# Kernel optimization log

Hardware: AMD Instinct MI355X
Metric: run time of the kernel (lower is better)

The kernel has to match this reference:

```python
import jax, jax.numpy as jnp
import numpy as np
import math

NUM_CLASSES = 80
ANCHORS = [(12.0, 16.0), (19.0, 36.0), (40.0, 28.0)]
ANGLES = [-np.pi/3, -np.pi/6, 0.0, np.pi/6, np.pi/3, np.pi/2]
STRIDE = 8.0
SCALE_XY = 1.05
IGNORE_THRESH = 0.5
MASKED_ANCHORS = np.array([[w/STRIDE, h/STRIDE, a] for (w, h) in ANCHORS for a in ANGLES], dtype=np.float32)  # [18,3]
NA = MASKED_ANCHORS.shape[0]
LAMBDA_COORD, LAMBDA_CONF, LAMBDA_CLS = 1.0, 10.0, 1.0
FOCAL_ALPHA, FOCAL_GAMMA = 0.25, 2.0


def setup_inputs() -> dict:
    key = jax.random.key(0)
    B, G, nT = 8, 76, 240
    k1, k2, k3, k4, k5, k6 = jax.random.split(key, 6)
    output = jax.random.normal(k1, (B, NA * (NUM_CLASSES + 6), G, G), jnp.float32) * 0.1
    tb = jax.random.randint(k2, (nT,), 0, B).astype(jnp.float32)
    tl = jax.random.randint(k3, (nT,), 0, NUM_CLASSES).astype(jnp.float32)
    txy = jax.random.uniform(k4, (nT, 2), minval=0.02, maxval=0.98)
    twh = jax.random.uniform(k5, (nT, 2), minval=0.05, maxval=0.4)
    tang = jax.random.uniform(k6, (nT, 1), minval=-np.pi/2, maxval=np.pi/2)
    target = jnp.concatenate([tb[:, None], tl[:, None], txy, twh, tang], axis=-1)  # [nT,7]
    return {"output": output, "target": target}


def _smooth_l1(x, y):
    d = jnp.abs(x - y)
    return jnp.where(d < 1.0, 0.5 * d * d, d - 0.5)


def _bce(p, t):
    eps = 1e-7
    p = jnp.clip(p, eps, 1.0 - eps)
    return -(t * jnp.log(p) + (1.0 - t) * jnp.log(1.0 - p))


def _focal(p, t):
    loss = _bce(p, t)
    p_t = t * p + (1.0 - t) * (1.0 - p)
    alpha_f = t * FOCAL_ALPHA + (1.0 - t) * (1.0 - FOCAL_ALPHA)
    return loss * alpha_f * (1.0 - p_t) ** FOCAL_GAMMA


def _ciou(pb, tb):
    # pb, tb: [N,5] (cx, cy, w, h, angle) in grid units
    p1, p2 = pb[:, :2] - pb[:, 2:4] / 2, pb[:, :2] + pb[:, 2:4] / 2
    t1, t2 = tb[:, :2] - tb[:, 2:4] / 2, tb[:, :2] + tb[:, 2:4] / 2
    w1, h1 = p2[:, 0] - p1[:, 0], p2[:, 1] - p1[:, 1]
    w2, h2 = t2[:, 0] - t1[:, 0], t2[:, 1] - t1[:, 1]
    area1, area2 = w1 * h1, w2 * h2
    c1, c2 = (p1 + p2) / 2, (t1 + t2) / 2
    inter = jnp.clip(jnp.minimum(p2, t2) - jnp.maximum(p1, t1), 0.0)
    inter_area = inter[:, 0] * inter[:, 1]
    inter_diag = jnp.sum((c2 - c1) ** 2, axis=-1)
    outer = jnp.clip(jnp.maximum(p2, t2) - jnp.minimum(p1, t1), 0.0)
    outer_diag = outer[:, 0] ** 2 + outer[:, 1] ** 2
    union = area1 + area2 - inter_area
    u = inter_diag / outer_diag
    iou = inter_area / union
    v = (4.0 / math.pi ** 2) * (jnp.arctan(w2 / h2) - jnp.arctan(w1 / h1)) ** 2
    alpha = jax.lax.stop_gradient(v / ((1.0 - iou) + v))
    ciou = jnp.clip(iou - (u + alpha * v), -1.0, 1.0)
    skew_iou = iou * jnp.abs(jnp.cos(pb[:, 4] - tb[:, 4]))
    return skew_iou, ciou


def _forward(output, target):
    B, G = output.shape[0], output.shape[2]
    nC = NUM_CLASSES
    ma = jnp.asarray(MASKED_ANCHORS)
    pred = output.reshape(B, NA, nC + 6, G, G).transpose(0, 1, 3, 4, 2)  # [B,A,G,G,C+6]
    px = jax.nn.sigmoid(pred[..., 0]) * SCALE_XY - (SCALE_XY - 1) / 2
    py = jax.nn.sigmoid(pred[..., 1]) * SCALE_XY - (SCALE_XY - 1) / 2
    pw, ph, pa = pred[..., 2], pred[..., 3], pred[..., 4]
    pconf = jax.nn.sigmoid(pred[..., 5])
    pcls = jax.nn.sigmoid(pred[..., 6:])
    gx = jnp.arange(G, dtype=output.dtype)[None, None, None, :]
    gy = jnp.arange(G, dtype=output.dtype)[None, None, :, None]
    aw = ma[:, 0].reshape(1, NA, 1, 1)
    ah = ma[:, 1].reshape(1, NA, 1, 1)
    aa = ma[:, 2].reshape(1, NA, 1, 1)
    pred_boxes = jnp.stack([px + gx, py + gy, jnp.exp(pw) * aw, jnp.exp(ph) * ah, pa + aa], axis=-1)  # [B,A,G,G,5]
    out_dec = jnp.concatenate([
        jnp.concatenate([pred_boxes[..., :4] * STRIDE, pred_boxes[..., 4:]], axis=-1).reshape(B, -1, 5),
        pconf.reshape(B, -1, 1),
        pcls.reshape(B, -1, nC)], axis=-1)

    # ---- build_targets ----
    tgt_boxes = jnp.concatenate([target[:, 2:6] * G, target[:, 6:]], axis=-1)  # [nT,5]
    gxy, gwh, ga = tgt_boxes[:, :2], tgt_boxes[:, 2:4], tgt_boxes[:, 4]
    aw_, ah_, aa_ = ma[:, 0][:, None], ma[:, 1][:, None], ma[:, 2][:, None]  # [A,1]
    w2, h2 = gwh[:, 0][None, :], gwh[:, 1][None, :]                          # [1,nT]
    inter = jnp.minimum(aw_, w2) * jnp.minimum(ah_, h2)
    union = aw_ * ah_ + 1e-16 + w2 * h2 - inter
    offset = jnp.abs(aa_ - ga[None, :])                                       # [A,nT]
    arious = (inter / union) * jnp.abs(jnp.cos(aa_ - ga[None, :]))            # [A,nT]
    best_n = jnp.argmax(arious, axis=0)                                       # [nT]
    b = target[:, 0].astype(jnp.int32)
    labels = target[:, 1].astype(jnp.int32)
    gi = gxy[:, 0].astype(jnp.int32)
    gj = gxy[:, 1].astype(jnp.int32)

    zeros = jnp.zeros((B, NA, G, G), output.dtype)
    obj = zeros.at[b, best_n, gj, gi].set(1.0)
    noobj = jnp.ones((B, NA, G, G), output.dtype)
    cond = (arious > IGNORE_THRESH) | ((arious > 0.4) & (offset < np.pi / 12))  # [A,nT]
    a_idx = jnp.broadcast_to(jnp.arange(NA)[:, None], arious.shape)
    bb = jnp.broadcast_to(b[None, :], arious.shape)
    gjb = jnp.broadcast_to(gj[None, :], arious.shape)
    gib = jnp.broadcast_to(gi[None, :], arious.shape)
    noobj = noobj.at[bb, a_idx, gjb, gib].min(jnp.where(cond, 0.0, 1.0))
    noobj = noobj.at[b, best_n, gj, gi].set(0.0)

    ta_grid = zeros.at[b, best_n, gj, gi].set(ga - ma[best_n, 2])
    tcls = jnp.zeros((B, NA, G, G, nC), output.dtype).at[b, best_n, gj, gi, labels].set(1.0)
    tconf = obj

    pb = pred_boxes[b, best_n, gj, gi]  # [nT,5]
    iou, ciou = _ciou(pb, tgt_boxes)
    img_size = STRIDE * G
    bbox_scale = jax.lax.stop_gradient(2.0 - gwh[:, 0] * gwh[:, 1] / img_size ** 2)
    ciou_t = bbox_scale * (1.0 - ciou)

    class_ok = (jnp.argmax(pcls[b, best_n, gj, gi], axis=-1) == labels).astype(output.dtype)
    class_mask = zeros.at[b, best_n, gj, gi].set(class_ok)
    iou_scores = zeros.at[b, best_n, gj, gi].set(iou)
    skew = zeros.at[b, best_n, gj, gi].set(jnp.exp(1.0 - iou) - 1.0)
    ciou_grid = zeros.at[b, best_n, gj, gi].set(ciou_t)

    # ---- losses (masked means replace boolean indexing) ----
    n_obj = jnp.maximum(jnp.sum(obj), 1.0)
    n_noobj = jnp.maximum(jnp.sum(noobj), 1.0)
    reg = _smooth_l1(pa, ta_grid) + ciou_grid
    reg_const = jax.lax.stop_gradient(skew / jnp.where(obj > 0, reg, 1.0))
    reg_loss = jnp.sum(reg * reg_const * obj) / n_obj
    fl = _focal(pconf, tconf)
    conf_loss = jnp.sum(fl * obj) / n_obj + jnp.sum(fl * noobj) / n_noobj
    cls_loss = jnp.sum(_bce(pcls, tcls) * obj[..., None]) / (n_obj * nC)
    total_loss = LAMBDA_COORD * reg_loss + LAMBDA_CONF * conf_loss + LAMBDA_CLS * cls_loss
    return out_dec, total_loss


def reference(output, target):
    return _forward(output, target)
```

## Files before the change

### kernel.cpp

```cpp
#include <hip/hip_runtime.h>
#include <math.h>

#define NCLS 80
#define NANC 18
#define NB 8
#define GG 76
#define SS (GG*GG)
#define CHN (NCLS+6)
#define NCELL (NB*NANC*SS)
#define FLAG_WORDS ((NCELL+31)/32)
#define NT_MAX 240
#define TILE 76
#define LSTR 77
#define TPB 4
#define TGRP (GG/TPB)
#define THR 512
#define NLOAD 4
#define TOT4 (CHN*(TILE/4))
#define NCONF4 (NCELL/4)
#define NCONFBLK ((NCONF4+255)/256)
#define PI_ 3.14159265358979323846

#define WS_WIN   64
#define WS_META  1024
#define WS_LM    4864
#define WS_FLAGS 6784

__device__ __constant__ float d_ma[NANC][3] = {
  {1.5f, 2.0f, (float)(-PI_/3)}, {1.5f, 2.0f, (float)(-PI_/6)}, {1.5f, 2.0f, 0.0f},
  {1.5f, 2.0f, (float)(PI_/6)},  {1.5f, 2.0f, (float)(PI_/3)},  {1.5f, 2.0f, (float)(PI_/2)},
  {2.375f, 4.5f, (float)(-PI_/3)}, {2.375f, 4.5f, (float)(-PI_/6)}, {2.375f, 4.5f, 0.0f},
  {2.375f, 4.5f, (float)(PI_/6)},  {2.375f, 4.5f, (float)(PI_/3)},  {2.375f, 4.5f, (float)(PI_/2)},
  {5.0f, 3.5f, (float)(-PI_/3)}, {5.0f, 3.5f, (float)(-PI_/6)}, {5.0f, 3.5f, 0.0f},
  {5.0f, 3.5f, (float)(PI_/6)},  {5.0f, 3.5f, (float)(PI_/3)},  {5.0f, 3.5f, (float)(PI_/2)},
};

__device__ __forceinline__ float sigm(float x) { return 1.0f / (1.0f + expf(-x)); }
__device__ __forceinline__ float fsig(float x) {
  return __builtin_amdgcn_rcpf(1.0f + __expf(-x));
}

__global__ __launch_bounds__(256) void k_prep(const float* __restrict__ tgt,
                                              unsigned* __restrict__ flags,
                                              int* __restrict__ win,
                                              int4* __restrict__ meta,
                                              uint2* __restrict__ lmout,
                                              int* __restrict__ cnt,
                                              double* __restrict__ acc, int nT) {
  __shared__ int s_key[NT_MAX], s_lab[NT_MAX];
  __shared__ int s_win[NT_MAX];
  __shared__ int s_zero;

  int t = threadIdx.x;
  uint4* f4 = (uint4*)flags;
  for (int i = t; i < FLAG_WORDS/4; i += 256) f4[i] = make_uint4(0,0,0,0);
  if (t < 4) { acc[t] = 0.0; cnt[t] = 0; }
  if (t == 0) s_zero = 0;
  __syncthreads();

  int bi = 0, gi = 0, gj = 0, bn = 0;
  unsigned cm = 0;
  if (t < nT) {
    float bf = tgt[t*7+0], lf = tgt[t*7+1];
    float gx = tgt[t*7+2] * (float)GG, gy = tgt[t*7+3] * (float)GG;
    float gw = tgt[t*7+4] * (float)GG, gh = tgt[t*7+5] * (float)GG;
    float ga = tgt[t*7+6];
    bi = (int)bf; gi = (int)gx; gj = (int)gy;
    int lab = (int)lf;
    float best = -1e30f;
    for (int a = 0; a < NANC; ++a) {
      float aw = d_ma[a][0], ah = d_ma[a][1], aa = d_ma[a][2];
      float inter = fminf(aw, gw) * fminf(ah, gh);
      float uni = aw*ah + 1e-16f + gw*gh - inter;
      float off = fabsf(aa - ga);
      float ar = inter / uni * fabsf(cosf(aa - ga));
      if (ar > best) { best = ar; bn = a; }
      if (ar > 0.5f || (ar > 0.4f && off < (float)(PI_/12))) cm |= (1u << a);
    }
    s_key[t] = ((bi*NANC + bn)*GG + gj)*GG + gi;
    s_lab[t] = lab;
    s_win[t] = 0;
  }
  __syncthreads();

  if (t < nT) {
    for (int a = 0; a < NANC; ++a) {
      if (((cm >> a) & 1u) || a == bn) {
        int cell = ((bi*NANC + a)*GG + gj)*GG + gi;
        unsigned bit = 1u << (cell & 31);
        unsigned old = atomicOr(&flags[cell >> 5], bit);
        if (!(old & bit)) atomicAdd(&s_zero, 1);
      }
    }
    int key = s_key[t];
    bool winner = true;
    for (int t2 = t + 1; t2 < nT; ++t2) if (s_key[t2] == key) { winner = false; break; }
    if (winner) {
      s_win[t] = 1;
      unsigned long long lm0 = 0, lm1 = 0;
      for (int t2 = 0; t2 < nT; ++t2) if (s_key[t2] == key) {
        int L = s_lab[t2];
        if (L < 64) lm0 |= 1ull << L; else lm1 |= 1ull << (L - 64);
      }
      lmout[t] = make_uint2((unsigned)(lm0 & 0xffffffffull), (unsigned)(lm0 >> 32));
      meta[t] = make_int4(bi, bn, gi, gj | ((int)(lm1 & 0xffffu) << 16));
      win[t] = 1;
    } else {
      win[t] = 0;
    }
  }
  __syncthreads();
  if (t == 0) {
    int nw = 0;
    for (int i = 0; i < nT; ++i) nw += s_win[i];
    cnt[0] = s_zero; cnt[1] = nw;
  }
}

__global__ __launch_bounds__(256) void k_loss(const float* __restrict__ tgt,
                                              const float* __restrict__ in,
                                              const int* __restrict__ win,
                                              const int4* __restrict__ meta,
                                              const uint2* __restrict__ lm,
                                              const unsigned* __restrict__ flags,
                                              double* __restrict__ acc,
                                              int* __restrict__ cnt,
                                              float* __restrict__ out, int nT) {
  int blk = blockIdx.x;
  int tid = threadIdx.x;
  int nblk = nT + NCONFBLK;

  if (blk < nT) {
    if (win[blk]) {
      int t = blk;
      int4 m = meta[t];
      int bi = m.x, bn = m.y, gi = m.z, gj = m.w & 0xffff;
      unsigned lmhi = ((unsigned)m.w) >> 16;
      uint2 l0 = lm[t];
      const float* base = in + ((size_t)(bi*NANC + bn)*CHN)*SS + (size_t)gj*GG + gi;

      float csum = 0.0f;
      if (tid < NCLS) {
        float p = fsig(base[(size_t)(6 + tid)*SS]);
        float pl = fminf(fmaxf(p, 1e-7f), 1.0f - 1e-7f);
        bool tc;
        if (tid < 32)      tc = (l0.x >> tid) & 1u;
        else if (tid < 64) tc = (l0.y >> (tid - 32)) & 1u;
        else               tc = (lmhi >> (tid - 64)) & 1u;
        csum = tc ? -__logf(pl) : -__logf(1.0f - pl);
      }
      for (int off = 32; off; off >>= 1) csum += __shfl_down(csum, off);
      if ((tid & 63) == 0 && tid < 128) atomicAdd(&acc[3], (double)csum);

      if (tid == 128) {
        float gx = tgt[t*7+2] * (float)GG, gyv = tgt[t*7+3] * (float)GG;
        float gw = tgt[t*7+4] * (float)GG, gh = tgt[t*7+5] * (float)GG;
        float ga = tgt[t*7+6];
        float rx = base[0], ry = base[(size_t)SS], rw = base[2*(size_t)SS],
              rh = base[3*(size_t)SS], ra = base[4*(size_t)SS], rcf = base[5*(size_t)SS];
        float aw = d_ma[bn][0], ah = d_ma[bn][1], aa = d_ma[bn][2];
        float px = sigm(rx)*1.05f - 0.025f + (float)gi;
        float py = sigm(ry)*1.05f - 0.025f + (float)gj;
        float pw = expf(rw)*aw, ph = expf(rh)*ah;
        float pang = ra + aa;
        float p1x = px - pw*0.5f, p1y = py - ph*0.5f, p2x = px + pw*0.5f, p2y = py + ph*0.5f;
        float t1x = gx - gw*0.5f, t1y = gyv - gh*0.5f, t2x = gx + gw*0.5f, t2y = gyv + gh*0.5f;
        float w1 = p2x - p1x, h1 = p2y - p1y, w2 = t2x - t1x, h2 = t2y - t1y;
        float area1 = w1*h1, area2 = w2*h2;
        float c1x = (p1x+p2x)*0.5f, c1y = (p1y+p2y)*0.5f, c2x = (t1x+t2x)*0.5f, c2y = (t1y+t2y)*0.5f;
        float ix = fmaxf(fminf(p2x,t2x) - fmaxf(p1x,t1x), 0.0f);
        float iy = fmaxf(fminf(p2y,t2y) - fmaxf(p1y,t1y), 0.0f);
        float inter_area = ix*iy;
        float dcx = c2x - c1x, dcy = c2y - c1y;
        float inter_diag = dcx*dcx + dcy*dcy;
        float ox = fmaxf(fmaxf(p2x,t2x) - fminf(p1x,t1x), 0.0f);
        float oy = fmaxf(fmaxf(p2y,t2y) - fminf(p1y,t1y), 0.0f);
        float outer_diag = ox*ox + oy*oy;
        float uni = area1 + area2 - inter_area;
        float u = inter_diag / outer_diag;
        float iou = inter_area / uni;
        float da = atanf(w2/h2) - atanf(w1/h1);
        float v = (float)(4.0/(PI_*PI_)) * da * da;
        float alpha = v / (1.0f - iou + v);
        float ciou = fminf(fmaxf(iou - (u + alpha*v), -1.0f), 1.0f);
        float skew_iou = iou * fabsf(cosf(pang - ga));
        float skew = expf(1.0f - skew_iou) - 1.0f;
        float bscale = 2.0f - gw*gh/369664.0f;
        float ciou_t = bscale * (1.0f - ciou);
        float ta = ga - aa;
        float d = fabsf(ra - ta);
        float sl1 = (d < 1.0f) ? 0.5f*d*d : d - 0.5f;
        float reg = sl1 + ciou_t;
        atomicAdd(&acc[2], (double)(reg * (skew / reg)));
        float pc = sigm(rcf);
        float pcl = fminf(fmaxf(pc, 1e-7f), 1.0f - 1e-7f);
        float om = 1.0f - pc;
        atomicAdd(&acc[1], (double)(-logf(pcl) * 0.25f * om * om));
      }
    }
  } else {
    __shared__ double wsum[4];
    int j = (blk - nT)*256 + tid;
    double fl = 0.0;
    if (j < NCONF4) {
      int ba = j / (SS/4);
      int q  = j - ba*(SS/4);
      int spos = 4*q;
      const float4 v4 = *(const float4*)(in + (size_t)ba*CHN*SS + 5*(size_t)SS + spos);
      int cell0 = ba*SS + spos;
      unsigned word = flags[cell0 >> 5];
      int bbit = cell0 & 31;
      float pv[4] = {v4.x, v4.y, v4.z, v4.w};
      #pragma unroll
      for (int e = 0; e < 4; ++e) {
        if (!((word >> (bbit + e)) & 1u)) {
          float p = fsig(pv[e]);
          float pcl = fminf(fmaxf(p, 1e-7f), 1.0f - 1e-7f);
          fl += (double)(-__logf(1.0f - pcl) * 0.75f * p * p);
        }
      }
    }
    int lane = tid & 63, wid = tid >> 6;
    for (int off = 32; off; off >>= 1) fl += __shfl_down(fl, off);
    if (lane == 0) wsum[wid] = fl;
    __syncthreads();
    if (tid == 0) {
      double s = wsum[0] + wsum[1] + wsum[2] + wsum[3];
      if (s != 0.0) atomicAdd(&acc[0], s);
    }
  }

  __syncthreads();
  if (tid == 0) {
    __threadfence();
    unsigned tk = atomicAdd((unsigned*)&cnt[2], 1u);
    if (tk == (unsigned)(nblk - 1)) {
      double a0 = atomicAdd(&acc[0], 0.0);
      double a1 = atomicAdd(&acc[1], 0.0);
      double a2 = atomicAdd(&acc[2], 0.0);
      double a3 = atomicAdd(&acc[3], 0.0);
      int c0 = atomicAdd(&cnt[0], 0);
      int c1 = atomicAdd(&cnt[1], 0);
      double n_obj = fmax((double)c1, 1.0);
      double n_noobj = fmax((double)(NCELL - c0), 1.0);
      double loss = a2/n_obj + 10.0*(a1/n_obj + a0/n_noobj) + a3/(n_obj*(double)NCLS);
      out[(size_t)NCELL*CHN] = (float)loss;
    }
  }
}

__global__ __launch_bounds__(THR) void k_main(const float* __restrict__ in,
                                              float* __restrict__ out) {
  __shared__ float lds[CHN * LSTR];
  int blk = blockIdx.x;
  int tgrp = blk % TGRP;
  int ba = blk / TGRP;
  int a = ba % NANC;
  float aw8 = d_ma[a][0]*8.0f, ah8 = d_ma[a][1]*8.0f, aa = d_ma[a][2];
  const float* plane_in = in + (size_t)ba*CHN*SS;
  float* plane_out = out + (size_t)ba*SS*CHN;
  int tile0 = tgrp*TPB;

  float4 r[NLOAD];
  { const float* tin = plane_in + tile0*TILE;
    #pragma unroll
    for (int k = 0; k < NLOAD; ++k) {
      int i = threadIdx.x + k*THR;
      if (i < TOT4) { int c = i/19, s4 = i - c*19;
        r[k] = *(const float4*)(tin + (size_t)c*SS + 4*s4); } }
  }

  for (int tt = 0; tt < TPB; ++tt) {
    int tile = tile0 + tt;
    __syncthreads();
    #pragma unroll
    for (int k = 0; k < NLOAD; ++k) {
      int i = threadIdx.x + k*THR;
      if (i < TOT4) {
        int c = i/19, s4 = i - c*19;
        float* p = &lds[c*LSTR + 4*s4];
        p[0] = r[k].x; p[1] = r[k].y; p[2] = r[k].z; p[3] = r[k].w;
      }
    }
    __syncthreads();
    if (tt + 1 < TPB) {
      const float* tin = plane_in + (tile + 1)*TILE;
      #pragma unroll
      for (int k = 0; k < NLOAD; ++k) {
        int i = threadIdx.x + k*THR;
        if (i < TOT4) { int c = i/19, s4 = i - c*19;
          r[k] = *(const float4*)(tin + (size_t)c*SS + 4*s4); } }
    }
    float gyf = (float)tile;
    float* orow = plane_out + (size_t)tile*TILE*CHN;
    for (int q = threadIdx.x; q < TILE*22; q += THR) {
      int s = q / 22;
      int j = q - s*22;
      int par = s & 1;
      if (j < 21) {
        int c = 2*par + 4*j;
        float v0 = lds[(c  )*LSTR + s];
        float v1 = lds[(c+1)*LSTR + s];
        float v2 = lds[(c+2)*LSTR + s];
        float v3 = lds[(c+3)*LSTR + s];
        float4 R;
        if (c >= 6) {
          R = make_float4(fsig(v0), fsig(v1), fsig(v2), fsig(v3));
        } else if (c == 0) {
          R.x = (fsig(v0)*1.05f - 0.025f + (float)s)*8.0f;
          R.y = (fsig(v1)*1.05f - 0.025f + gyf)*8.0f;
          R.z = __expf(v2)*aw8;
          R.w = __expf(v3)*ah8;
        } else if (c == 4) {
          R.x = v0 + aa;
          R.y = fsig(v1);
          R.z = fsig(v2);
          R.w = fsig(v3);
        } else {
          R.x = __expf(v0)*aw8;
          R.y = __expf(v1)*ah8;
          R.z = v2 + aa;
          R.w = fsig(v3);
        }
        *(float4*)(orow + s*CHN + c) = R;
      } else {
        int c = par ? 0 : 84;
        float v0 = lds[(c  )*LSTR + s];
        float v1 = lds[(c+1)*LSTR + s];
        float2 R;
        if (par) {
          R.x = (fsig(v0)*1.05f - 0.025f + (float)s)*8.0f;
          R.y = (fsig(v1)*1.05f - 0.025f + gyf)*8.0f;
        } else {
          R = make_float2(fsig(v0), fsig(v1));
        }
        *(float2*)(orow + s*CHN + c) = R;
      }
    }
  }
}

extern "C" void kernel_launch(void* const* d_in, const int* in_sizes, int n_in,
                              void* d_out, int out_size, void* d_ws, size_t ws_size,
                              hipStream_t stream) {
  const float* in  = (const float*)d_in[0];
  const float* tgt = (const float*)d_in[1];
  float* out = (float*)d_out;
  double* acc = (double*)d_ws;
  int* cnt = (int*)((char*)d_ws + 32);
  int* win = (int*)((char*)d_ws + WS_WIN);
  int4* meta = (int4*)((char*)d_ws + WS_META);
  uint2* lm = (uint2*)((char*)d_ws + WS_LM);
  unsigned* flags = (unsigned*)((char*)d_ws + WS_FLAGS);
  int nT = in_sizes[1] / 7;
  if (nT > NT_MAX) nT = NT_MAX;

  hipLaunchKernelGGL(k_prep, dim3(1), dim3(256), 0, stream,
                     tgt, flags, win, meta, lm, cnt, acc, nT);
  hipLaunchKernelGGL(k_loss, dim3(nT + NCONFBLK), dim3(256), 0, stream,
                     tgt, in, win, meta, lm, flags, acc, cnt, out, nT);
  hipLaunchKernelGGL(k_main, dim3(NB*NANC*TGRP), dim3(THR), 0, stream, in, out);
}
```

Measured before the change: 217.0 us.

## Fuse loss and decode kernels into one launch with nontemporal stores

Merges the loss kernel and the main decode/transpose kernel into one grid, with the first blocks doing loss work and the rest doing the transposed decode, so one launch and its tail gap go away. The decode part now runs 256 threads per block with 7 loads per thread instead of 512 with 4, and output stores use nontemporal hints. Loss blocks now reserve the large LDS array even though they do not use it, which can lower their occupancy.

```diff
diff --git a/kernel.cpp b/kernel.cpp
--- a/kernel.cpp
+++ b/kernel.cpp
@@ -14,9 +14,10 @@
 #define LSTR 77
 #define TPB 4
 #define TGRP (GG/TPB)
-#define THR 512
-#define NLOAD 4
+#define THR 256
+#define NLOAD 7
 #define TOT4 (CHN*(TILE/4))
+#define NTRANS (NB*NANC*TGRP)
 #define NCONF4 (NCELL/4)
 #define NCONFBLK ((NCONF4+255)/256)
 #define PI_ 3.14159265358979323846
@@ -25,6 +26,9 @@
 #define WS_META  1024
 #define WS_LM    4864
 #define WS_FLAGS 6784
+
+typedef float fx4 __attribute__((ext_vector_type(4)));
+typedef float fx2 __attribute__((ext_vector_type(2)));
 
 __device__ __constant__ float d_ma[NANC][3] = {
   {1.5f, 2.0f, (float)(-PI_/3)}, {1.5f, 2.0f, (float)(-PI_/6)}, {1.5f, 2.0f, 0.0f},
@@ -117,144 +121,144 @@
   }
 }
 
-__global__ __launch_bounds__(256) void k_loss(const float* __restrict__ tgt,
-                                              const float* __restrict__ in,
-                                              const int* __restrict__ win,
-                                              const int4* __restrict__ meta,
-                                              const uint2* __restrict__ lm,
-                                              const unsigned* __restrict__ flags,
-                                              double* __restrict__ acc,
-                                              int* __restrict__ cnt,
-                                              float* __restrict__ out, int nT) {
+__global__ __launch_bounds__(THR) void k_fused(const float* __restrict__ in,
+                                               float* __restrict__ out,
+                                               const unsigned* __restrict__ flags,
+                                               const float* __restrict__ tgt,
+                                               const int* __restrict__ win,
+                                               const int4* __restrict__ meta,
+                                               const uint2* __restrict__ lm,
+                                               double* __restrict__ acc,
+                                               int* __restrict__ cnt,
+                                               int nT) {
+  __shared__ float lds[CHN * LSTR];
+  int nloss = nT + NCONFBLK;
   int blk = blockIdx.x;
   int tid = threadIdx.x;
-  int nblk = nT + NCONFBLK;
-
-  if (blk < nT) {
-    if (win[blk]) {
-      int t = blk;
-      int4 m = meta[t];
-      int bi = m.x, bn = m.y, gi = m.z, gj = m.w & 0xffff;
-      unsigned lmhi = ((unsigned)m.w) >> 16;
-      uint2 l0 = lm[t];
-      const float* base = in + ((size_t)(bi*NANC + bn)*CHN)*SS + (size_t)gj*GG + gi;
-
-      float csum = 0.0f;
-      if (tid < NCLS) {
-        float p = fsig(base[(size_t)(6 + tid)*SS]);
-        float pl = fminf(fmaxf(p, 1e-7f), 1.0f - 1e-7f);
-        bool tc;
-        if (tid < 32)      tc = (l0.x >> tid) & 1u;
-        else if (tid < 64) tc = (l0.y >> (tid - 32)) & 1u;
-        else               tc = (lmhi >> (tid - 64)) & 1u;
-        csum = tc ? -__logf(pl) : -__logf(1.0f - pl);
-      }
-      for (int off = 32; off; off >>= 1) csum += __shfl_down(csum, off);
-      if ((tid & 63) == 0 && tid < 128) atomicAdd(&acc[3], (double)csum);
-
-      if (tid == 128) {
-        float gx = tgt[t*7+2] * (float)GG, gyv = tgt[t*7+3] * (float)GG;
-        float gw = tgt[t*7+4] * (float)GG, gh = tgt[t*7+5] * (float)GG;
-        float ga = tgt[t*7+6];
-        float rx = base[0], ry = base[(size_t)SS], rw = base[2*(size_t)SS],
-              rh = base[3*(size_t)SS], ra = base[4*(size_t)SS], rcf = base[5*(size_t)SS];
-        float aw = d_ma[bn][0], ah = d_ma[bn][1], aa = d_ma[bn][2];
-        float px = sigm(rx)*1.05f - 0.025f + (float)gi;
-        float py = sigm(ry)*1.05f - 0.025f + (float)gj;
-        float pw = expf(rw)*aw, ph = expf(rh)*ah;
-        float pang = ra + aa;
-        float p1x = px - pw*0.5f, p1y = py - ph*0.5f, p2x = px + pw*0.5f, p2y = py + ph*0.5f;
-        float t1x = gx - gw*0.5f, t1y = gyv - gh*0.5f, t2x = gx + gw*0.5f, t2y = gyv + gh*0.5f;
-        float w1 = p2x - p1x, h1 = p2y - p1y, w2 = t2x - t1x, h2 = t2y - t1y;
-        float area1 = w1*h1, area2 = w2*h2;
-        float c1x = (p1x+p2x)*0.5f, c1y = (p1y+p2y)*0.5f, c2x = (t1x+t2x)*0.5f, c2y = (t1y+t2y)*0.5f;
-        float ix = fmaxf(fminf(p2x,t2x) - fmaxf(p1x,t1x), 0.0f);
-        float iy = fmaxf(fminf(p2y,t2y) - fmaxf(p1y,t1y), 0.0f);
-        float inter_area = ix*iy;
-        float dcx = c2x - c1x, dcy = c2y - c1y;
-        float inter_diag = dcx*dcx + dcy*dcy;
-        float ox = fmaxf(fmaxf(p2x,t2x) - fminf(p1x,t1x), 0.0f);
-        float oy = fmaxf(fmaxf(p2y,t2y) - fminf(p1y,t1y), 0.0f);
-        float outer_diag = ox*ox + oy*oy;
-        float uni = area1 + area2 - inter_area;
-        float u = inter_diag / outer_diag;
-        float iou = inter_area / uni;
-        float da = atanf(w2/h2) - atanf(w1/h1);
-        float v = (float)(4.0/(PI_*PI_)) * da * da;
-        float alpha = v / (1.0f - iou + v);
-        float ciou = fminf(fmaxf(iou - (u + alpha*v), -1.0f), 1.0f);
-        float skew_iou = iou * fabsf(cosf(pang - ga));
-        float skew = expf(1.0f - skew_iou) - 1.0f;
-        float bscale = 2.0f - gw*gh/369664.0f;
-        float ciou_t = bscale * (1.0f - ciou);
-        float ta = ga - aa;
-        float d = fabsf(ra - ta);
-        float sl1 = (d < 1.0f) ? 0.5f*d*d : d - 0.5f;
-        float reg = sl1 + ciou_t;
-        atomicAdd(&acc[2], (double)(reg * (skew / reg)));
-        float pc = sigm(rcf);
-        float pcl = fminf(fmaxf(pc, 1e-7f), 1.0f - 1e-7f);
-        float om = 1.0f - pc;
-        atomicAdd(&acc[1], (double)(-logf(pcl) * 0.25f * om * om));
-      }
-    }
-  } else {
-    __shared__ double wsum[4];
-    int j = (blk - nT)*256 + tid;
-    double fl = 0.0;
-    if (j < NCONF4) {
-      int ba = j / (SS/4);
-      int q  = j - ba*(SS/4);
-      int spos = 4*q;
-      const float4 v4 = *(const float4*)(in + (size_t)ba*CHN*SS + 5*(size_t)SS + spos);
-      int cell0 = ba*SS + spos;
-      unsigned word = flags[cell0 >> 5];
-      int bbit = cell0 & 31;
-      float pv[4] = {v4.x, v4.y, v4.z, v4.w};
-      #pragma unroll
-      for (int e = 0; e < 4; ++e) {
-        if (!((word >> (bbit + e)) & 1u)) {
-          float p = fsig(pv[e]);
-          float pcl = fminf(fmaxf(p, 1e-7f), 1.0f - 1e-7f);
-          fl += (double)(-__logf(1.0f - pcl) * 0.75f * p * p);
-        }
-      }
-    }
-    int lane = tid & 63, wid = tid >> 6;
-    for (int off = 32; off; off >>= 1) fl += __shfl_down(fl, off);
-    if (lane == 0) wsum[wid] = fl;
+
+  if (blk < nloss) {
+    if (blk < nT) {
+      if (win[blk]) {
+        int t = blk;
+        int4 m = meta[t];
+        int bi = m.x, bn = m.y, gi = m.z, gj = m.w & 0xffff;
+        unsigned lmhi = ((unsigned)m.w) >> 16;
+        uint2 l0 = lm[t];
+        const float* base = in + ((size_t)(bi*NANC + bn)*CHN)*SS + (size_t)gj*GG + gi;
+
+        float csum = 0.0f;
+        if (tid < NCLS) {
+          float p = fsig(base[(size_t)(6 + tid)*SS]);
+          float pl = fminf(fmaxf(p, 1e-7f), 1.0f - 1e-7f);
+          bool tc;
+          if (tid < 32)      tc = (l0.x >> tid) & 1u;
+          else if (tid < 64) tc = (l0.y >> (tid - 32)) & 1u;
+          else               tc = (lmhi >> (tid - 64)) & 1u;
+          csum = tc ? -__logf(pl) : -__logf(1.0f - pl);
+        }
+        for (int off = 32; off; off >>= 1) csum += __shfl_down(csum, off);
+        if ((tid & 63) == 0 && tid < 128) atomicAdd(&acc[3], (double)csum);
+
+        if (tid == 128) {
+          float gx = tgt[t*7+2] * (float)GG, gyv = tgt[t*7+3] * (float)GG;
+          float gw = tgt[t*7+4] * (float)GG, gh = tgt[t*7+5] * (float)GG;
+          float ga = tgt[t*7+6];
+          float rx = base[0], ry = base[(size_t)SS], rw = base[2*(size_t)SS],
+                rh = base[3*(size_t)SS], ra = base[4*(size_t)SS], rcf = base[5*(size_t)SS];
+          float aw = d_ma[bn][0], ah = d_ma[bn][1], aa = d_ma[bn][2];
+          float px = sigm(rx)*1.05f - 0.025f + (float)gi;
+          float py = sigm(ry)*1.05f - 0.025f + (float)gj;
+          float pw = expf(rw)*aw, ph = expf(rh)*ah;
+          float pang = ra + aa;
+          float p1x = px - pw*0.5f, p1y = py - ph*0.5f, p2x = px + pw*0.5f, p2y = py + ph*0.5f;
+          float t1x = gx - gw*0.5f, t1y = gyv - gh*0.5f, t2x = gx + gw*0.5f, t2y = gyv + gh*0.5f;
+          float w1 = p2x - p1x, h1 = p2y - p1y, w2 = t2x - t1x, h2 = t2y - t1y;
+          float area1 = w1*h1, area2 = w2*h2;
+          float c1x = (p1x+p2x)*0.5f, c1y = (p1y+p2y)*0.5f, c2x = (t1x+t2x)*0.5f, c2y = (t1y+t2y)*0.5f;
+          float ix = fmaxf(fminf(p2x,t2x) - fmaxf(p1x,t1x), 0.0f);
+          float iy = fmaxf(fminf(p2y,t2y) - fmaxf(p1y,t1y), 0.0f);
+          float inter_area = ix*iy;
+          float dcx = c2x - c1x, dcy = c2y - c1y;
+          float inter_diag = dcx*dcx + dcy*dcy;
+          float ox = fmaxf(fmaxf(p2x,t2x) - fminf(p1x,t1x), 0.0f);
+          float oy = fmaxf(fmaxf(p2y,t2y) - fminf(p1y,t1y), 0.0f);
+          float outer_diag = ox*ox + oy*oy;
+          float uni = area1 + area2 - inter_area;
+          float u = inter_diag / outer_diag;
+          float iou = inter_area / uni;
+          float da = atanf(w2/h2) - atanf(w1/h1);
+          float v = (float)(4.0/(PI_*PI_)) * da * da;
+          float alpha = v / (1.0f - iou + v);
+          float ciou = fminf(fmaxf(iou - (u + alpha*v), -1.0f), 1.0f);
+          float skew_iou = iou * fabsf(cosf(pang - ga));
+          float skew = expf(1.0f - skew_iou) - 1.0f;
+          float bscale = 2.0f - gw*gh/369664.0f;
+          float ciou_t = bscale * (1.0f - ciou);
+          float ta = ga - aa;
+          float d = fabsf(ra - ta);
+          float sl1 = (d < 1.0f) ? 0.5f*d*d : d - 0.5f;
+          float reg = sl1 + ciou_t;
+          atomicAdd(&acc[2], (double)(reg * (skew / reg)));
+          float pc = sigm(rcf);
+          float pcl = fminf(fmaxf(pc, 1e-7f), 1.0f - 1e-7f);
+          float om = 1.0f - pc;
+          atomicAdd(&acc[1], (double)(-logf(pcl) * 0.25f * om * om));
+        }
+      }
+    } else {
+      __shared__ double wsum[4];
+      int j = (blk - nT)*256 + tid;
+      double fl = 0.0;
+      if (j < NCONF4) {
+        int ba = j / (SS/4);
+        int q  = j - ba*(SS/4);
+        int spos = 4*q;
+        const float4 v4 = *(const float4*)(in + (size_t)ba*CHN*SS + 5*(size_t)SS + spos);
+        int cell0 = ba*SS + spos;
+        unsigned word = flags[cell0 >> 5];
+        int bbit = cell0 & 31;
+        float pv[4] = {v4.x, v4.y, v4.z, v4.w};
+        #pragma unroll
+        for (int e = 0; e < 4; ++e) {
+          if (!((word >> (bbit + e)) & 1u)) {
+            float p = fsig(pv[e]);
+            float pcl = fminf(fmaxf(p, 1e-7f), 1.0f - 1e-7f);
+            fl += (double)(-__logf(1.0f - pcl) * 0.75f * p * p);
+          }
+        }
+      }
+      int lane = tid & 63, wid = tid >> 6;
+      for (int off = 32; off; off >>= 1) fl += __shfl_down(fl, off);
+      if (lane == 0) wsum[wid] = fl;
+      __syncthreads();
+      if (tid == 0) {
+        double s = wsum[0] + wsum[1] + wsum[2] + wsum[3];
+        if (s != 0.0) atomicAdd(&acc[0], s);
+      }
+    }
     __syncthreads();
     if (tid == 0) {
-      double s = wsum[0] + wsum[1] + wsum[2] + wsum[3];
-      if (s != 0.0) atomicAdd(&acc[0], s);
-    }
-  }
-
-  __syncthreads();
-  if (tid == 0) {
-    __threadfence();
-    unsigned tk = atomicAdd((unsigned*)&cnt[2], 1u);
-    if (tk == (unsigned)(nblk - 1)) {
-      double a0 = atomicAdd(&acc[0], 0.0);
-      double a1 = atomicAdd(&acc[1], 0.0);
-      double a2 = atomicAdd(&acc[2], 0.0);
-      double a3 = atomicAdd(&acc[3], 0.0);
-      int c0 = atomicAdd(&cnt[0], 0);
-      int c1 = atomicAdd(&cnt[1], 0);
-      double n_obj = fmax((double)c1, 1.0);
-      double n_noobj = fmax((double)(NCELL - c0), 1.0);
-      double loss = a2/n_obj + 10.0*(a1/n_obj + a0/n_noobj) + a3/(n_obj*(double)NCLS);
-      out[(size_t)NCELL*CHN] = (float)loss;
-    }
-  }
-}
-
-__global__ __launch_bounds__(THR) void k_main(const float* __restrict__ in,
-                                              float* __restrict__ out) {
-  __shared__ float lds[CHN * LSTR];
-  int blk = blockIdx.x;
-  int tgrp = blk % TGRP;
-  int ba = blk / TGRP;
+      __threadfence();
+      unsigned tk = atomicAdd((unsigned*)&cnt[2], 1u);
+      if (tk == (unsigned)(nloss - 1)) {
+        double a0 = atomicAdd(&acc[0], 0.0);
+        double a1 = atomicAdd(&acc[1], 0.0);
+        double a2 = atomicAdd(&acc[2], 0.0);
+        double a3 = atomicAdd(&acc[3], 0.0);
+        int c0 = atomicAdd(&cnt[0], 0);
+        int c1 = atomicAdd(&cnt[1], 0);
+        double n_obj = fmax((double)c1, 1.0);
+        double n_noobj = fmax((double)(NCELL - c0), 1.0);
+        double loss = a2/n_obj + 10.0*(a1/n_obj + a0/n_noobj) + a3/(n_obj*(double)NCLS);
+        out[(size_t)NCELL*CHN] = (float)loss;
+      }
+    }
+    return;
+  }
+
+  int tblk = blk - nloss;
+  int tgrp = tblk % TGRP;
+  int ba = tblk / TGRP;
   int a = ba % NANC;
   float aw8 = d_ma[a][0]*8.0f, ah8 = d_ma[a][1]*8.0f, aa = d_ma[a][2];
   const float* plane_in = in + (size_t)ba*CHN*SS;
@@ -303,9 +307,9 @@
         float v1 = lds[(c+1)*LSTR + s];
         float v2 = lds[(c+2)*LSTR + s];
         float v3 = lds[(c+3)*LSTR + s];
-        float4 R;
+        fx4 R;
         if (c >= 6) {
-          R = make_float4(fsig(v0), fsig(v1), fsig(v2), fsig(v3));
+          R.x = fsig(v0); R.y = fsig(v1); R.z = fsig(v2); R.w = fsig(v3);
         } else if (c == 0) {
           R.x = (fsig(v0)*1.05f - 0.025f + (float)s)*8.0f;
           R.y = (fsig(v1)*1.05f - 0.025f + gyf)*8.0f;
@@ -322,19 +326,19 @@
           R.z = v2 + aa;
           R.w = fsig(v3);
         }
-        *(float4*)(orow + s*CHN + c) = R;
+        __builtin_nontemporal_store(R, (fx4*)(orow + s*CHN + c));
       } else {
         int c = par ? 0 : 84;
         float v0 = lds[(c  )*LSTR + s];
         float v1 = lds[(c+1)*LSTR + s];
-        float2 R;
+        fx2 R;
         if (par) {
           R.x = (fsig(v0)*1.05f - 0.025f + (float)s)*8.0f;
           R.y = (fsig(v1)*1.05f - 0.025f + gyf)*8.0f;
         } else {
-          R = make_float2(fsig(v0), fsig(v1));
-        }
-        *(float2*)(orow + s*CHN + c) = R;
+          R.x = fsig(v0); R.y = fsig(v1);
+        }
+        __builtin_nontemporal_store(R, (fx2*)(orow + s*CHN + c));
       }
     }
   }
@@ -357,7 +361,6 @@
 
   hipLaunchKernelGGL(k_prep, dim3(1), dim3(256), 0, stream,
                      tgt, flags, win, meta, lm, cnt, acc, nT);
-  hipLaunchKernelGGL(k_loss, dim3(nT + NCONFBLK), dim3(256), 0, stream,
-                     tgt, in, win, meta, lm, flags, acc, cnt, out, nT);
-  hipLaunchKernelGGL(k_main, dim3(NB*NANC*TGRP), dim3(THR), 0, stream, in, out);
+  hipLaunchKernelGGL(k_fused, dim3(nT + NCONFBLK + NTRANS), dim3(THR), 0, stream,
+                     in, out, flags, tgt, win, meta, lm, acc, cnt, nT);
 }
```

New measurement: 223.5 us. +3.0%, slower.
